# Kernel optimization log

Measured on AMD Instinct MI355X. Metric: run time of the kernel, lower is better.

Reference implementation:

```python
import jax, jax.numpy as jnp
import numpy as np

N_PATHS, SEQ_LEN = 8192, 512
DATA_DIM, HIDDEN = 2, 128
MIN_VOL, MAX_VOL = 1e-4, 5.0


def setup_inputs() -> dict:
    key = jax.random.key(0)
    ks = jax.random.split(key, 10)
    def w(k, fin, fout, scale=1.0):
        return (jax.random.normal(k, (fin, fout), jnp.float32) * (scale / np.sqrt(fin))).astype(jnp.float32)
    # diffusion output bias init from the torch module: log(exp(target_vol) - 1 + 1e-8)
    gb3_init = float(np.log(np.exp(0.1) - 1.0 + 1e-8))
    return {
        "y0": jax.random.normal(ks[0], (N_PATHS, DATA_DIM), jnp.float32) * 0.1,
        "ts": jnp.arange(SEQ_LEN, dtype=jnp.float32),  # dt = 1.0 between outputs
        "dW": jax.random.normal(ks[1], (SEQ_LEN - 1, N_PATHS, DATA_DIM), jnp.float32),
        "fw1": w(ks[2], DATA_DIM + 1, HIDDEN), "fb1": jnp.zeros((HIDDEN,), jnp.float32),
        "fw2": w(ks[3], HIDDEN, HIDDEN),       "fb2": jnp.zeros((HIDDEN,), jnp.float32),
        "fw3": w(ks[4], HIDDEN, DATA_DIM, 0.02), "fb3": jnp.zeros((DATA_DIM,), jnp.float32),
        "gw1": w(ks[5], DATA_DIM, HIDDEN),     "gb1": jnp.zeros((HIDDEN,), jnp.float32),
        "gw2": w(ks[6], HIDDEN, HIDDEN),       "gb2": jnp.zeros((HIDDEN,), jnp.float32),
        "gw3": w(ks[7], HIDDEN, DATA_DIM, 0.02),
        "gb3": jnp.full((DATA_DIM,), gb3_init, jnp.float32),
    }


def _sde_paths(y0, ts, dW, fw1, fb1, fw2, fb2, fw3, fb3, gw1, gb1, gw2, gb2, gw3, gb3):
    def drift(y):  # f(t, y): MLP on [y, spread]
        spread = y[:, 0:1] - y[:, 1:2]
        h = jnp.concatenate([y, spread], axis=-1)            # [N, D+1]
        h = jax.nn.silu(h @ fw1 + fb1)
        h = jax.nn.silu(h @ fw2 + fb2)
        return h @ fw3 + fb3                                  # [N, D]

    def diffusion(y):  # g(t, y): softplus + clamp
        h = jax.nn.silu(y @ gw1 + gb1)
        h = jax.nn.silu(h @ gw2 + gb2)
        raw = h @ gw3 + gb3
        return jnp.clip(jax.nn.softplus(raw), MIN_VOL, MAX_VOL)  # [N, D]

    dts = ts[1:] - ts[:-1]  # [T-1]

    def step(y, inp):
        dw_std, dt = inp
        dw = dw_std * jnp.sqrt(dt)                 # Brownian increment ~ N(0, dt)
        f = drift(y)
        g, vjp_g = jax.vjp(diffusion, y)
        v = 0.5 * (dw * dw - dt)                   # Milstein weight (Ito)
        corr = vjp_g(v * g)[0]                     # torchsde autograd gdg_prod
        y1 = y + f * dt + g * dw + corr
        return y1, y1

    _, ys = jax.lax.scan(step, y0, (dW, dts))      # ys: [T-1, N, D]
    paths = jnp.concatenate([y0[None], ys], axis=0)  # [T, N, D]
    return jnp.transpose(paths, (1, 0, 2))           # [N, T, D]


def reference(y0, ts, dW, fw1, fb1, fw2, fb2, fw3, fb3, gw1, gb1, gw2, gb2, gw3, gb3):
    return _sde_paths(y0, ts, dW, fw1, fb1, fw2, fb2, fw3, fb3,
                      gw1, gb1, gw2, gb2, gw3, gb3)
```

## Files before the change

kernel.cpp:

```cpp
#include <hip/hip_runtime.h>
#include <math.h>

#define H      128
#define NPATH  8192
#define TLEN   512
#define BP     32
#define NTHR   512

typedef short bf16x8 __attribute__((ext_vector_type(8)));
typedef float f32x4  __attribute__((ext_vector_type(4)));

#define MFMA(a,b,c) __builtin_amdgcn_mfma_f32_16x16x32_bf16((a),(b),(c),0,0,0)

#define O_WF2T  0
#define O_WG2T  (O_WF2T + 32768)
#define O_WG2R  (O_WG2T + 32768)
#define O_BFH   (O_WG2R + 32768)
#define O_BFL   (O_BFH + 8192)
#define O_BGH   (O_BFL + 8192)
#define O_BGL   (O_BGH + 8192)
#define O_PF    (O_BGL + 8192)
#define O_PRAW  (O_PF   + 1024)
#define O_PCORR (O_PRAW + 1024)
#define O_TS    (O_PCORR+ 1024)
#define SMEM_BYTES (O_TS + TLEN*4)

__device__ __forceinline__ float bf2f(unsigned v){ return __uint_as_float(v << 16); }
__device__ __forceinline__ unsigned short f2bf(float f){
  unsigned u = __float_as_uint(f);
  return (unsigned short)((u + 0x7fffu + ((u >> 16) & 1u)) >> 16);
}
__device__ __forceinline__ float ldany(const void* p, long long i, bool isbf){
  return isbf ? bf2f(((const unsigned short*)p)[i]) : ((const float*)p)[i];
}
__device__ __forceinline__ unsigned short ldbf(const void* p, long long i, bool isbf){
  return isbf ? ((const unsigned short*)p)[i] : f2bf(((const float*)p)[i]);
}
__device__ __forceinline__ float fsig(float x){
  return __builtin_amdgcn_rcpf(1.0f + __expf(-x));
}
__device__ __forceinline__ float fsilu(float x){ return x * fsig(x); }
__device__ __forceinline__ float fsilud(float x){
  float s = fsig(x); return s * (1.0f + x * (1.0f - s));
}
__device__ __forceinline__ float fsoftplus(float x){
  if (x > 15.0f) return x;
  return __logf(1.0f + __expf(x));
}
__device__ __forceinline__ void split2(float x, unsigned short& hi, unsigned short& lo){
  unsigned short h = f2bf(x);
  hi = h;
  lo = f2bf(x - bf2f(h));
}
__device__ __forceinline__ int physB(int row, int col){
  return (row << 8) + ((((col >> 3) ^ (row & 15)) << 4) | ((col & 7) << 1));
}
__device__ __forceinline__ bf16x8 ldfrag(const char* base, int row, int col){
  union { uint4 u; bf16x8 b; } v;
  v.u = *(const uint4*)(base + physB(row, col));
  return v.b;
}
__device__ __forceinline__ void st8(char* base, int row, int col, const unsigned short h[8]){
  uint4 u = make_uint4((unsigned)h[0] | ((unsigned)h[1] << 16),
                       (unsigned)h[2] | ((unsigned)h[3] << 16),
                       (unsigned)h[4] | ((unsigned)h[5] << 16),
                       (unsigned)h[6] | ((unsigned)h[7] << 16));
  *(uint4*)(base + physB(row, col)) = u;
}
__device__ __forceinline__ void st4(char* base, int row, int col, const unsigned short h[4]){
  uint2 u = make_uint2((unsigned)h[0] | ((unsigned)h[1] << 16),
                       (unsigned)h[2] | ((unsigned)h[3] << 16));
  *(uint2*)(base + physB(row, col)) = u;
}

__global__ __launch_bounds__(NTHR, 2)
void GeneratorSDE_kernel(const void* __restrict__ y0, const void* __restrict__ ts,
                         const void* __restrict__ dW,
                         const void* __restrict__ fw1, const void* __restrict__ fb1,
                         const void* __restrict__ fw2, const void* __restrict__ fb2,
                         const void* __restrict__ fw3, const void* __restrict__ fb3,
                         const void* __restrict__ gw1, const void* __restrict__ gb1,
                         const void* __restrict__ gw2, const void* __restrict__ gb2,
                         const void* __restrict__ gw3, const void* __restrict__ gb3,
                         void* __restrict__ out)
{
  extern __shared__ char sm[];
  const int tid  = threadIdx.x;
  const int lane = tid & 63;
  const int w    = tid >> 6;
  const int wp   = w >> 1;
  const int nt   = w & 1;
  const int m16  = lane & 15;
  const int q    = lane >> 4;
  const int gpb  = blockIdx.x * BP;
  const int p1   = nt*16 + m16;
  const int gp   = gpb + p1;
  const int k8   = wp*32 + q*8;

  const bool isbf = (((const unsigned*)ts)[1] != 0x3f800000u);

  for (int e = tid; e < H * H; e += NTHR){
    int k = e >> 7, n = e & 127;
    unsigned short fv = ldbf(fw2, e, isbf);
    unsigned short gv = ldbf(gw2, e, isbf);
    *(unsigned short*)(sm + O_WF2T + physB(n, k)) = fv;
    *(unsigned short*)(sm + O_WG2T + physB(n, k)) = gv;
    *(unsigned short*)(sm + O_WG2R + physB(k, n)) = gv;
  }
  for (int e = tid; e < TLEN; e += NTHR)
    ((float*)(sm + O_TS))[e] = ldany(ts, e, isbf);

  float w3f0[8], w3f1[8], w3g0[8], w3g1[8], gw1b0[8], gw1b1[8], gb1b[8], fb2r[8], gb2r[8];
  #pragma unroll
  for (int i = 0; i < 8; ++i){
    int nr = 32*wp + ((i >> 2) << 4) + (q << 2) + (i & 3);
    w3f0[i]  = ldany(fw3, 2*nr + 0, isbf);
    w3f1[i]  = ldany(fw3, 2*nr + 1, isbf);
    w3g0[i]  = ldany(gw3, 2*nr + 0, isbf);
    w3g1[i]  = ldany(gw3, 2*nr + 1, isbf);
    gw1b0[i] = ldany(gw1, nr,       isbf);
    gw1b1[i] = ldany(gw1, H + nr,   isbf);
    gb1b[i]  = ldany(gb1, nr,       isbf);
    fb2r[i]  = ldany(fb2, nr,       isbf);
    gb2r[i]  = ldany(gb2, nr,       isbf);
  }
  float fw1r0[8], fw1r1[8], fw1r2[8], fb1r[8], gw1r0[8], gw1r1[8], gb1r[8];
  #pragma unroll
  for (int kk = 0; kk < 8; ++kk){
    int k = k8 + kk;
    fw1r0[kk] = ldany(fw1, k,       isbf);
    fw1r1[kk] = ldany(fw1, H + k,   isbf);
    fw1r2[kk] = ldany(fw1, 2*H + k, isbf);
    fb1r[kk]  = ldany(fb1, k,       isbf);
    gw1r0[kk] = ldany(gw1, k,       isbf);
    gw1r1[kk] = ldany(gw1, H + k,   isbf);
    gb1r[kk]  = ldany(gb1, k,       isbf);
  }
  const float fb3r0 = ldany(fb3, 0, isbf), fb3r1 = ldany(fb3, 1, isbf);
  const float gb3r0 = ldany(gb3, 0, isbf), gb3r1 = ldany(gb3, 1, isbf);

  float ycur0 = ldany(y0, (long long)gp*2 + 0, isbf);
  float ycur1 = ldany(y0, (long long)gp*2 + 1, isbf);
  if (w < 2 && lane < 16){
    size_t r = (size_t)gp * TLEN;
    if (isbf) ((unsigned*)out)[r] = (unsigned)f2bf(ycur0) | ((unsigned)f2bf(ycur1) << 16);
    else      ((float2*)out)[r]   = make_float2(ycur0, ycur1);
  }
  float2 dwcur;
  {
    long long e = (long long)gp * 2;
    if (isbf){ unsigned u = *(const unsigned*)((const unsigned short*)dW + e);
               dwcur = make_float2(bf2f(u & 0xffffu), bf2f(u >> 16)); }
    else       dwcur = *(const float2*)((const float*)dW + e);
  }
  __syncthreads();

  const float* TSf = (const float*)(sm + O_TS);

  for (int t = 0; t < TLEN - 1; ++t){
    float dt = TSf[t+1] - TSf[t];
    float sqdt = sqrtf(dt);

    float2 dwnext;
    {
      int tn = (t + 1 <= TLEN - 2) ? t + 1 : TLEN - 2;
      long long e = ((long long)tn * NPATH + gp) * 2;
      if (isbf){ unsigned u = *(const unsigned*)((const unsigned short*)dW + e);
                 dwnext = make_float2(bf2f(u & 0xffffu), bf2f(u >> 16)); }
      else       dwnext = *(const float2*)((const float*)dW + e);
    }

    {
      float ysp = ycur0 - ycur1;
      unsigned short fh[8], fl[8], gh[8], gl[8];
      #pragma unroll
      for (int kk = 0; kk < 8; ++kk){
        float hf = fsilu(fb1r[kk] + ycur0*fw1r0[kk] + ycur1*fw1r1[kk] + ysp*fw1r2[kk]);
        float hg = fsilu(gb1r[kk] + ycur0*gw1r0[kk] + ycur1*gw1r1[kk]);
        split2(hf, fh[kk], fl[kk]);
        split2(hg, gh[kk], gl[kk]);
      }
      st8(sm + O_BFH, p1, k8, fh);
      st8(sm + O_BFL, p1, k8, fl);
      st8(sm + O_BGH, p1, k8, gh);
      st8(sm + O_BGL, p1, k8, gl);
    }
    __syncthreads();

    f32x4 accg[2];
    {
      f32x4 accf[2];
      accf[0] = (f32x4)0.f; accf[1] = (f32x4)0.f;
      accg[0] = (f32x4)0.f; accg[1] = (f32x4)0.f;
      #pragma unroll
      for (int kt = 0; kt < 4; ++kt){
        int colk = kt*32 + q*8;
        bf16x8 af0 = ldfrag(sm + O_WF2T, 32*wp + m16,      colk);
        bf16x8 af1 = ldfrag(sm + O_WF2T, 32*wp + 16 + m16, colk);
        bf16x8 bfh = ldfrag(sm + O_BFH, p1, colk);
        bf16x8 bfl = ldfrag(sm + O_BFL, p1, colk);
        accf[0] = MFMA(af0, bfl, accf[0]); accf[0] = MFMA(af0, bfh, accf[0]);
        accf[1] = MFMA(af1, bfl, accf[1]); accf[1] = MFMA(af1, bfh, accf[1]);
        bf16x8 ag0 = ldfrag(sm + O_WG2T, 32*wp + m16,      colk);
        bf16x8 ag1 = ldfrag(sm + O_WG2T, 32*wp + 16 + m16, colk);
        bf16x8 bgh = ldfrag(sm + O_BGH, p1, colk);
        bf16x8 bgl = ldfrag(sm + O_BGL, p1, colk);
        accg[0] = MFMA(ag0, bgl, accg[0]); accg[0] = MFMA(ag0, bgh, accg[0]);
        accg[1] = MFMA(ag1, bgl, accg[1]); accg[1] = MFMA(ag1, bgh, accg[1]);
      }
      float pf0 = 0, pf1 = 0, pr0 = 0, pr1 = 0;
      #pragma unroll
      for (int mi = 0; mi < 2; ++mi)
        #pragma unroll
        for (int r = 0; r < 4; ++r){
          int i = mi*4 + r;
          float vf = fsilu(accf[mi][r] + fb2r[i]);
          pf0 += vf * w3f0[i];
          pf1 += vf * w3f1[i];
          float zg = accg[mi][r] + gb2r[i];
          accg[mi][r] = zg;
          float vg = fsilu(zg);
          pr0 += vg * w3g0[i];
          pr1 += vg * w3g1[i];
        }
      pf0 += __shfl_xor(pf0, 16, 64); pf0 += __shfl_xor(pf0, 32, 64);
      pf1 += __shfl_xor(pf1, 16, 64); pf1 += __shfl_xor(pf1, 32, 64);
      pr0 += __shfl_xor(pr0, 16, 64); pr0 += __shfl_xor(pr0, 32, 64);
      pr1 += __shfl_xor(pr1, 16, 64); pr1 += __shfl_xor(pr1, 32, 64);
      if (lane < 16){
        *(float2*)(sm + O_PF   + (wp*32 + p1)*8) = make_float2(pf0, pf1);
        *(float2*)(sm + O_PRAW + (wp*32 + p1)*8) = make_float2(pr0, pr1);
      }
    }
    __syncthreads();

    float g0, g1, dw0, dw1, cr0, cr1;
    {
      float raw0 = gb3r0, raw1 = gb3r1;
      #pragma unroll
      for (int w2 = 0; w2 < 4; ++w2){
        float2 v = *(const float2*)(sm + O_PRAW + (w2*32 + p1)*8);
        raw0 += v.x; raw1 += v.y;
      }
      dw0 = dwcur.x * sqdt; dw1 = dwcur.y * sqdt;
      float vv0 = 0.5f*(dw0*dw0 - dt), vv1 = 0.5f*(dw1*dw1 - dt);
      float sp0 = fsoftplus(raw0), sp1 = fsoftplus(raw1);
      g0 = fminf(fmaxf(sp0, 1e-4f), 5.0f);
      g1 = fminf(fmaxf(sp1, 1e-4f), 5.0f);
      float m0 = (sp0 > 1e-4f && sp0 < 5.0f) ? 1.0f : 0.0f;
      float m1 = (sp1 > 1e-4f && sp1 < 5.0f) ? 1.0f : 0.0f;
      cr0 = vv0 * (g0 * fsig(raw0) * m0);
      cr1 = vv1 * (g1 * fsig(raw1) * m1);
    }

    #pragma unroll
    for (int mi = 0; mi < 2; ++mi){
      unsigned short hi[4], lo[4];
      #pragma unroll
      for (int r = 0; r < 4; ++r){
        int i = mi*4 + r;
        float c2 = (cr0 * w3g0[i] + cr1 * w3g1[i]) * fsilud(accg[mi][r]);
        split2(c2, hi[r], lo[r]);
      }
      st4(sm + O_BFH, p1, 32*wp + 16*mi + q*4, hi);
      st4(sm + O_BFL, p1, 32*wp + 16*mi + q*4, lo);
    }
    __syncthreads();

    {
      f32x4 accc[2];
      accc[0] = (f32x4)0.f; accc[1] = (f32x4)0.f;
      #pragma unroll
      for (int kt = 0; kt < 4; ++kt){
        int colk = kt*32 + q*8;
        bf16x8 a0 = ldfrag(sm + O_WG2R, 32*wp + m16,      colk);
        bf16x8 a1 = ldfrag(sm + O_WG2R, 32*wp + 16 + m16, colk);
        bf16x8 bh = ldfrag(sm + O_BFH, p1, colk);
        bf16x8 bl = ldfrag(sm + O_BFL, p1, colk);
        accc[0] = MFMA(a0, bl, accc[0]); accc[0] = MFMA(a0, bh, accc[0]);
        accc[1] = MFMA(a1, bl, accc[1]); accc[1] = MFMA(a1, bh, accc[1]);
      }
      float pc0 = 0, pc1 = 0;
      #pragma unroll
      for (int mi = 0; mi < 2; ++mi)
        #pragma unroll
        for (int r = 0; r < 4; ++r){
          int i = mi*4 + r;
          float z1 = gb1b[i] + ycur0*gw1b0[i] + ycur1*gw1b1[i];
          float u  = accc[mi][r] * fsilud(z1);
          pc0 += u * gw1b0[i];
          pc1 += u * gw1b1[i];
        }
      pc0 += __shfl_xor(pc0, 16, 64); pc0 += __shfl_xor(pc0, 32, 64);
      pc1 += __shfl_xor(pc1, 16, 64); pc1 += __shfl_xor(pc1, 32, 64);
      if (lane < 16)
        *(float2*)(sm + O_PCORR + (wp*32 + p1)*8) = make_float2(pc0, pc1);
    }
    __syncthreads();

    {
      float f0 = fb3r0, f1 = fb3r1, c0 = 0.f, c1 = 0.f;
      #pragma unroll
      for (int w2 = 0; w2 < 4; ++w2){
        float2 a = *(const float2*)(sm + O_PF    + (w2*32 + p1)*8);
        float2 b = *(const float2*)(sm + O_PCORR + (w2*32 + p1)*8);
        f0 += a.x; f1 += a.y; c0 += b.x; c1 += b.y;
      }
      ycur0 += f0*dt + g0*dw0 + c0;
      ycur1 += f1*dt + g1*dw1 + c1;
      if (w < 2 && lane < 16){
        size_t r = (size_t)gp * TLEN + (t + 1);
        if (isbf) ((unsigned*)out)[r] = (unsigned)f2bf(ycur0) | ((unsigned)f2bf(ycur1) << 16);
        else      ((float2*)out)[r]   = make_float2(ycur0, ycur1);
      }
      dwcur = dwnext;
    }
  }
}

extern "C" void kernel_launch(void* const* d_in, const int* in_sizes, int n_in,
                              void* d_out, int out_size, void* d_ws, size_t ws_size,
                              hipStream_t stream)
{
  (void)in_sizes; (void)n_in; (void)out_size; (void)d_ws; (void)ws_size;
  hipFuncSetAttribute((const void*)GeneratorSDE_kernel,
                      hipFuncAttributeMaxDynamicSharedMemorySize, SMEM_BYTES);
  GeneratorSDE_kernel<<<dim3(NPATH / BP), dim3(NTHR), SMEM_BYTES, stream>>>(
      d_in[0], d_in[1], d_in[2],
      d_in[3], d_in[4], d_in[5], d_in[6], d_in[7], d_in[8],
      d_in[9], d_in[10], d_in[11], d_in[12], d_in[13], d_in[14],
      d_out);
}
```

Measured before the change: 2.066 ms.

## Software-pipeline two path halves across phases with register-resident weight fragments

Splits each block's 32 paths into two 16-path halves and interleaves their per-step phases, so the MFMA work of one half overlaps the elementwise work of the other. Each of the 8 waves now owns a 16-row slice of the hidden dimension, which lets the layer-2 weight fragments be loaded into registers once instead of re-read from LDS every step. The layer-1 work is split across waves by network (drift or diffusion), and the bf16 hi/lo split now uses truncation with packed stores. The price is more register pressure, a trickier cross-half schedule, and truncation instead of round-to-nearest for the hi part.

```diff
diff --git a/kernel.cpp b/kernel.cpp
--- a/kernel.cpp
+++ b/kernel.cpp
@@ -13,16 +13,16 @@
 #define MFMA(a,b,c) __builtin_amdgcn_mfma_f32_16x16x32_bf16((a),(b),(c),0,0,0)
 
 #define O_WF2T  0
-#define O_WG2T  (O_WF2T + 32768)
-#define O_WG2R  (O_WG2T + 32768)
-#define O_BFH   (O_WG2R + 32768)
-#define O_BFL   (O_BFH + 8192)
-#define O_BGH   (O_BFL + 8192)
-#define O_BGL   (O_BGH + 8192)
-#define O_PF    (O_BGL + 8192)
-#define O_PRAW  (O_PF   + 1024)
-#define O_PCORR (O_PRAW + 1024)
-#define O_TS    (O_PCORR+ 1024)
+#define O_WG2T  32768
+#define O_WG2R  65536
+#define O_BFH   98304
+#define O_BFL   106496
+#define O_BGH   114688
+#define O_BGL   122880
+#define O_PF    131072
+#define O_PRAW  133120
+#define O_PCORR 135168
+#define O_TS    137216
 #define SMEM_BYTES (O_TS + TLEN*4)
 
 __device__ __forceinline__ float bf2f(unsigned v){ return __uint_as_float(v << 16); }
@@ -47,10 +47,13 @@
   if (x > 15.0f) return x;
   return __logf(1.0f + __expf(x));
 }
-__device__ __forceinline__ void split2(float x, unsigned short& hi, unsigned short& lo){
-  unsigned short h = f2bf(x);
-  hi = h;
-  lo = f2bf(x - bf2f(h));
+__device__ __forceinline__ void splitpk(float x0, float x1, unsigned& hipk, unsigned& lopk){
+  unsigned u0 = __float_as_uint(x0), u1 = __float_as_uint(x1);
+  unsigned h0 = u0 & 0xffff0000u, h1 = u1 & 0xffff0000u;
+  hipk = (u0 >> 16) | h1;
+  float l0 = x0 - __uint_as_float(h0);
+  float l1 = x1 - __uint_as_float(h1);
+  lopk = (__float_as_uint(l0) >> 16) | (__float_as_uint(l1) & 0xffff0000u);
 }
 __device__ __forceinline__ int physB(int row, int col){
   return (row << 8) + ((((col >> 3) ^ (row & 15)) << 4) | ((col & 7) << 1));
@@ -59,18 +62,6 @@
   union { uint4 u; bf16x8 b; } v;
   v.u = *(const uint4*)(base + physB(row, col));
   return v.b;
-}
-__device__ __forceinline__ void st8(char* base, int row, int col, const unsigned short h[8]){
-  uint4 u = make_uint4((unsigned)h[0] | ((unsigned)h[1] << 16),
-                       (unsigned)h[2] | ((unsigned)h[3] << 16),
-                       (unsigned)h[4] | ((unsigned)h[5] << 16),
-                       (unsigned)h[6] | ((unsigned)h[7] << 16));
-  *(uint4*)(base + physB(row, col)) = u;
-}
-__device__ __forceinline__ void st4(char* base, int row, int col, const unsigned short h[4]){
-  uint2 u = make_uint2((unsigned)h[0] | ((unsigned)h[1] << 16),
-                       (unsigned)h[2] | ((unsigned)h[3] << 16));
-  *(uint2*)(base + physB(row, col)) = u;
 }
 
 __global__ __launch_bounds__(NTHR, 2)
@@ -88,14 +79,11 @@
   const int tid  = threadIdx.x;
   const int lane = tid & 63;
   const int w    = tid >> 6;
-  const int wp   = w >> 1;
-  const int nt   = w & 1;
   const int m16  = lane & 15;
   const int q    = lane >> 4;
   const int gpb  = blockIdx.x * BP;
-  const int p1   = nt*16 + m16;
-  const int gp   = gpb + p1;
-  const int k8   = wp*32 + q*8;
+  const int net  = w & 1;
+  const int k8   = (w >> 1)*32 + q*8;
 
   const bool isbf = (((const unsigned*)ts)[1] != 0x3f800000u);
 
@@ -110,211 +98,221 @@
   for (int e = tid; e < TLEN; e += NTHR)
     ((float*)(sm + O_TS))[e] = ldany(ts, e, isbf);
 
-  float w3f0[8], w3f1[8], w3g0[8], w3g1[8], gw1b0[8], gw1b1[8], gb1b[8], fb2r[8], gb2r[8];
-  #pragma unroll
-  for (int i = 0; i < 8; ++i){
-    int nr = 32*wp + ((i >> 2) << 4) + (q << 2) + (i & 3);
-    w3f0[i]  = ldany(fw3, 2*nr + 0, isbf);
-    w3f1[i]  = ldany(fw3, 2*nr + 1, isbf);
-    w3g0[i]  = ldany(gw3, 2*nr + 0, isbf);
-    w3g1[i]  = ldany(gw3, 2*nr + 1, isbf);
-    gw1b0[i] = ldany(gw1, nr,       isbf);
-    gw1b1[i] = ldany(gw1, H + nr,   isbf);
-    gb1b[i]  = ldany(gb1, nr,       isbf);
-    fb2r[i]  = ldany(fb2, nr,       isbf);
-    gb2r[i]  = ldany(gb2, nr,       isbf);
-  }
-  float fw1r0[8], fw1r1[8], fw1r2[8], fb1r[8], gw1r0[8], gw1r1[8], gb1r[8];
+  float w3f0[4], w3f1[4], w3g0[4], w3g1[4], fb2r[4], gb2r[4], gw1b0[4], gw1b1[4], gb1b[4];
+  #pragma unroll
+  for (int r = 0; r < 4; ++r){
+    int nr = 16*w + (q << 2) + r;
+    w3f0[r]  = ldany(fw3, 2*nr + 0, isbf);
+    w3f1[r]  = ldany(fw3, 2*nr + 1, isbf);
+    w3g0[r]  = ldany(gw3, 2*nr + 0, isbf);
+    w3g1[r]  = ldany(gw3, 2*nr + 1, isbf);
+    gw1b0[r] = ldany(gw1, nr,       isbf);
+    gw1b1[r] = ldany(gw1, H + nr,   isbf);
+    gb1b[r]  = ldany(gb1, nr,       isbf);
+    fb2r[r]  = ldany(fb2, nr,       isbf);
+    gb2r[r]  = ldany(gb2, nr,       isbf);
+  }
+  float wr0[8], wr1[8], wr2[8], brg[8];
   #pragma unroll
   for (int kk = 0; kk < 8; ++kk){
     int k = k8 + kk;
-    fw1r0[kk] = ldany(fw1, k,       isbf);
-    fw1r1[kk] = ldany(fw1, H + k,   isbf);
-    fw1r2[kk] = ldany(fw1, 2*H + k, isbf);
-    fb1r[kk]  = ldany(fb1, k,       isbf);
-    gw1r0[kk] = ldany(gw1, k,       isbf);
-    gw1r1[kk] = ldany(gw1, H + k,   isbf);
-    gb1r[kk]  = ldany(gb1, k,       isbf);
+    if (net == 0){
+      wr0[kk] = ldany(fw1, k,       isbf);
+      wr1[kk] = ldany(fw1, H + k,   isbf);
+      wr2[kk] = ldany(fw1, 2*H + k, isbf);
+      brg[kk] = ldany(fb1, k,       isbf);
+    } else {
+      wr0[kk] = ldany(gw1, k,       isbf);
+      wr1[kk] = ldany(gw1, H + k,   isbf);
+      wr2[kk] = 0.0f;
+      brg[kk] = ldany(gb1, k,       isbf);
+    }
   }
   const float fb3r0 = ldany(fb3, 0, isbf), fb3r1 = ldany(fb3, 1, isbf);
   const float gb3r0 = ldany(gb3, 0, isbf), gb3r1 = ldany(gb3, 1, isbf);
 
-  float ycur0 = ldany(y0, (long long)gp*2 + 0, isbf);
-  float ycur1 = ldany(y0, (long long)gp*2 + 1, isbf);
-  if (w < 2 && lane < 16){
-    size_t r = (size_t)gp * TLEN;
-    if (isbf) ((unsigned*)out)[r] = (unsigned)f2bf(ycur0) | ((unsigned)f2bf(ycur1) << 16);
-    else      ((float2*)out)[r]   = make_float2(ycur0, ycur1);
-  }
-  float2 dwcur;
-  {
+  float2 yc[2], dwc[2], dwn[2], gS[2], dwS[2];
+  f32x4  az[2];
+  #pragma unroll
+  for (int h = 0; h < 2; ++h){
+    int gp = gpb + 16*h + m16;
+    yc[h].x = ldany(y0, (long long)gp*2 + 0, isbf);
+    yc[h].y = ldany(y0, (long long)gp*2 + 1, isbf);
     long long e = (long long)gp * 2;
     if (isbf){ unsigned u = *(const unsigned*)((const unsigned short*)dW + e);
-               dwcur = make_float2(bf2f(u & 0xffffu), bf2f(u >> 16)); }
-    else       dwcur = *(const float2*)((const float*)dW + e);
+               dwc[h] = make_float2(bf2f(u & 0xffffu), bf2f(u >> 16)); }
+    else       dwc[h] = *(const float2*)((const float*)dW + e);
+    dwn[h] = dwc[h]; gS[h] = make_float2(0.f,0.f); dwS[h] = make_float2(0.f,0.f);
+    az[h] = (f32x4)0.f;
+  }
+  #pragma unroll
+  for (int h = 0; h < 2; ++h){
+    if (w == h && lane < 16){
+      size_t r = (size_t)(gpb + 16*h + lane) * TLEN;
+      if (isbf) ((unsigned*)out)[r] = (unsigned)f2bf(yc[h].x) | ((unsigned)f2bf(yc[h].y) << 16);
+      else      ((float2*)out)[r]   = make_float2(yc[h].x, yc[h].y);
+    }
   }
   __syncthreads();
 
+  bf16x8 afr[4], agr[4], abr[4];
+  #pragma unroll
+  for (int kt = 0; kt < 4; ++kt){
+    int colk = kt*32 + q*8;
+    afr[kt] = ldfrag(sm + O_WF2T, 16*w + m16, colk);
+    agr[kt] = ldfrag(sm + O_WG2T, 16*w + m16, colk);
+    abr[kt] = ldfrag(sm + O_WG2R, 16*w + m16, colk);
+  }
+
   const float* TSf = (const float*)(sm + O_TS);
-
-  for (int t = 0; t < TLEN - 1; ++t){
-    float dt = TSf[t+1] - TSf[t];
-    float sqdt = sqrtf(dt);
-
-    float2 dwnext;
-    {
-      int tn = (t + 1 <= TLEN - 2) ? t + 1 : TLEN - 2;
-      long long e = ((long long)tn * NPATH + gp) * 2;
-      if (isbf){ unsigned u = *(const unsigned*)((const unsigned short*)dW + e);
-                 dwnext = make_float2(bf2f(u & 0xffffu), bf2f(u >> 16)); }
-      else       dwnext = *(const float2*)((const float*)dW + e);
-    }
-
-    {
-      float ysp = ycur0 - ycur1;
-      unsigned short fh[8], fl[8], gh[8], gl[8];
-      #pragma unroll
-      for (int kk = 0; kk < 8; ++kk){
-        float hf = fsilu(fb1r[kk] + ycur0*fw1r0[kk] + ycur1*fw1r1[kk] + ysp*fw1r2[kk]);
-        float hg = fsilu(gb1r[kk] + ycur0*gw1r0[kk] + ycur1*gw1r1[kk]);
-        split2(hf, fh[kk], fl[kk]);
-        split2(hg, gh[kk], gl[kk]);
-      }
-      st8(sm + O_BFH, p1, k8, fh);
-      st8(sm + O_BFL, p1, k8, fl);
-      st8(sm + O_BGH, p1, k8, gh);
-      st8(sm + O_BGL, p1, k8, gl);
-    }
-    __syncthreads();
-
-    f32x4 accg[2];
-    {
-      f32x4 accf[2];
-      accf[0] = (f32x4)0.f; accf[1] = (f32x4)0.f;
-      accg[0] = (f32x4)0.f; accg[1] = (f32x4)0.f;
-      #pragma unroll
-      for (int kt = 0; kt < 4; ++kt){
-        int colk = kt*32 + q*8;
-        bf16x8 af0 = ldfrag(sm + O_WF2T, 32*wp + m16,      colk);
-        bf16x8 af1 = ldfrag(sm + O_WF2T, 32*wp + 16 + m16, colk);
-        bf16x8 bfh = ldfrag(sm + O_BFH, p1, colk);
-        bf16x8 bfl = ldfrag(sm + O_BFL, p1, colk);
-        accf[0] = MFMA(af0, bfl, accf[0]); accf[0] = MFMA(af0, bfh, accf[0]);
-        accf[1] = MFMA(af1, bfl, accf[1]); accf[1] = MFMA(af1, bfh, accf[1]);
-        bf16x8 ag0 = ldfrag(sm + O_WG2T, 32*wp + m16,      colk);
-        bf16x8 ag1 = ldfrag(sm + O_WG2T, 32*wp + 16 + m16, colk);
-        bf16x8 bgh = ldfrag(sm + O_BGH, p1, colk);
-        bf16x8 bgl = ldfrag(sm + O_BGL, p1, colk);
-        accg[0] = MFMA(ag0, bgl, accg[0]); accg[0] = MFMA(ag0, bgh, accg[0]);
-        accg[1] = MFMA(ag1, bgl, accg[1]); accg[1] = MFMA(ag1, bgh, accg[1]);
-      }
-      float pf0 = 0, pf1 = 0, pr0 = 0, pr1 = 0;
-      #pragma unroll
-      for (int mi = 0; mi < 2; ++mi)
-        #pragma unroll
-        for (int r = 0; r < 4; ++r){
-          int i = mi*4 + r;
-          float vf = fsilu(accf[mi][r] + fb2r[i]);
-          pf0 += vf * w3f0[i];
-          pf1 += vf * w3f1[i];
-          float zg = accg[mi][r] + gb2r[i];
-          accg[mi][r] = zg;
-          float vg = fsilu(zg);
-          pr0 += vg * w3g0[i];
-          pr1 += vg * w3g1[i];
-        }
-      pf0 += __shfl_xor(pf0, 16, 64); pf0 += __shfl_xor(pf0, 32, 64);
-      pf1 += __shfl_xor(pf1, 16, 64); pf1 += __shfl_xor(pf1, 32, 64);
-      pr0 += __shfl_xor(pr0, 16, 64); pr0 += __shfl_xor(pr0, 32, 64);
-      pr1 += __shfl_xor(pr1, 16, 64); pr1 += __shfl_xor(pr1, 32, 64);
-      if (lane < 16){
-        *(float2*)(sm + O_PF   + (wp*32 + p1)*8) = make_float2(pf0, pf1);
-        *(float2*)(sm + O_PRAW + (wp*32 + p1)*8) = make_float2(pr0, pr1);
-      }
-    }
-    __syncthreads();
-
-    float g0, g1, dw0, dw1, cr0, cr1;
-    {
-      float raw0 = gb3r0, raw1 = gb3r1;
-      #pragma unroll
-      for (int w2 = 0; w2 < 4; ++w2){
-        float2 v = *(const float2*)(sm + O_PRAW + (w2*32 + p1)*8);
-        raw0 += v.x; raw1 += v.y;
-      }
-      dw0 = dwcur.x * sqdt; dw1 = dwcur.y * sqdt;
-      float vv0 = 0.5f*(dw0*dw0 - dt), vv1 = 0.5f*(dw1*dw1 - dt);
-      float sp0 = fsoftplus(raw0), sp1 = fsoftplus(raw1);
-      g0 = fminf(fmaxf(sp0, 1e-4f), 5.0f);
-      g1 = fminf(fmaxf(sp1, 1e-4f), 5.0f);
-      float m0 = (sp0 > 1e-4f && sp0 < 5.0f) ? 1.0f : 0.0f;
-      float m1 = (sp1 > 1e-4f && sp1 < 5.0f) ? 1.0f : 0.0f;
-      cr0 = vv0 * (g0 * fsig(raw0) * m0);
-      cr1 = vv1 * (g1 * fsig(raw1) * m1);
-    }
-
-    #pragma unroll
-    for (int mi = 0; mi < 2; ++mi){
-      unsigned short hi[4], lo[4];
-      #pragma unroll
-      for (int r = 0; r < 4; ++r){
-        int i = mi*4 + r;
-        float c2 = (cr0 * w3g0[i] + cr1 * w3g1[i]) * fsilud(accg[mi][r]);
-        split2(c2, hi[r], lo[r]);
-      }
-      st4(sm + O_BFH, p1, 32*wp + 16*mi + q*4, hi);
-      st4(sm + O_BFL, p1, 32*wp + 16*mi + q*4, lo);
-    }
-    __syncthreads();
-
-    {
-      f32x4 accc[2];
-      accc[0] = (f32x4)0.f; accc[1] = (f32x4)0.f;
-      #pragma unroll
-      for (int kt = 0; kt < 4; ++kt){
-        int colk = kt*32 + q*8;
-        bf16x8 a0 = ldfrag(sm + O_WG2R, 32*wp + m16,      colk);
-        bf16x8 a1 = ldfrag(sm + O_WG2R, 32*wp + 16 + m16, colk);
-        bf16x8 bh = ldfrag(sm + O_BFH, p1, colk);
-        bf16x8 bl = ldfrag(sm + O_BFL, p1, colk);
-        accc[0] = MFMA(a0, bl, accc[0]); accc[0] = MFMA(a0, bh, accc[0]);
-        accc[1] = MFMA(a1, bl, accc[1]); accc[1] = MFMA(a1, bh, accc[1]);
-      }
-      float pc0 = 0, pc1 = 0;
-      #pragma unroll
-      for (int mi = 0; mi < 2; ++mi)
-        #pragma unroll
-        for (int r = 0; r < 4; ++r){
-          int i = mi*4 + r;
-          float z1 = gb1b[i] + ycur0*gw1b0[i] + ycur1*gw1b1[i];
-          float u  = accc[mi][r] * fsilud(z1);
-          pc0 += u * gw1b0[i];
-          pc1 += u * gw1b1[i];
-        }
-      pc0 += __shfl_xor(pc0, 16, 64); pc0 += __shfl_xor(pc0, 32, 64);
-      pc1 += __shfl_xor(pc1, 16, 64); pc1 += __shfl_xor(pc1, 32, 64);
-      if (lane < 16)
-        *(float2*)(sm + O_PCORR + (wp*32 + p1)*8) = make_float2(pc0, pc1);
-    }
-    __syncthreads();
-
-    {
+  float dtprev = 1.0f, dtcur = 1.0f, sqcur = 1.0f;
+
+  auto P0 = [&](int h, int c){
+    if (c > 0){
       float f0 = fb3r0, f1 = fb3r1, c0 = 0.f, c1 = 0.f;
       #pragma unroll
-      for (int w2 = 0; w2 < 4; ++w2){
-        float2 a = *(const float2*)(sm + O_PF    + (w2*32 + p1)*8);
-        float2 b = *(const float2*)(sm + O_PCORR + (w2*32 + p1)*8);
+      for (int w2 = 0; w2 < 8; ++w2){
+        float2 a = *(const float2*)(sm + O_PF    + (w2*32 + 16*h + m16)*8);
+        float2 b = *(const float2*)(sm + O_PCORR + (w2*32 + 16*h + m16)*8);
         f0 += a.x; f1 += a.y; c0 += b.x; c1 += b.y;
       }
-      ycur0 += f0*dt + g0*dw0 + c0;
-      ycur1 += f1*dt + g1*dw1 + c1;
-      if (w < 2 && lane < 16){
-        size_t r = (size_t)gp * TLEN + (t + 1);
-        if (isbf) ((unsigned*)out)[r] = (unsigned)f2bf(ycur0) | ((unsigned)f2bf(ycur1) << 16);
-        else      ((float2*)out)[r]   = make_float2(ycur0, ycur1);
+      yc[h].x += f0*dtprev + gS[h].x*dwS[h].x + c0;
+      yc[h].y += f1*dtprev + gS[h].y*dwS[h].y + c1;
+      if (w == h && lane < 16){
+        size_t r = (size_t)(gpb + 16*h + lane) * TLEN + c;
+        if (isbf) ((unsigned*)out)[r] = (unsigned)f2bf(yc[h].x) | ((unsigned)f2bf(yc[h].y) << 16);
+        else      ((float2*)out)[r]   = make_float2(yc[h].x, yc[h].y);
       }
-      dwcur = dwnext;
-    }
+    }
+    if (c < TLEN - 1){
+      int tn = (c + 1 <= TLEN - 2) ? c + 1 : TLEN - 2;
+      long long e = ((long long)tn * NPATH + (gpb + 16*h + m16)) * 2;
+      if (isbf){ unsigned u = *(const unsigned*)((const unsigned short*)dW + e);
+                 dwn[h] = make_float2(bf2f(u & 0xffffu), bf2f(u >> 16)); }
+      else       dwn[h] = *(const float2*)((const float*)dW + e);
+
+      float ya = yc[h].x, yb = yc[h].y, ysp = ya - yb;
+      float v[8];
+      #pragma unroll
+      for (int kk = 0; kk < 8; ++kk)
+        v[kk] = fsilu(brg[kk] + ya*wr0[kk] + yb*wr1[kk] + ysp*wr2[kk]);
+      unsigned hp[4], lp[4];
+      splitpk(v[0], v[1], hp[0], lp[0]);
+      splitpk(v[2], v[3], hp[1], lp[1]);
+      splitpk(v[4], v[5], hp[2], lp[2]);
+      splitpk(v[6], v[7], hp[3], lp[3]);
+      char* bh = sm + (net ? O_BGH : O_BFH);
+      char* bl = sm + (net ? O_BGL : O_BFL);
+      int off = physB(16*h + m16, k8);
+      *(uint4*)(bh + off) = make_uint4(hp[0], hp[1], hp[2], hp[3]);
+      *(uint4*)(bl + off) = make_uint4(lp[0], lp[1], lp[2], lp[3]);
+    }
+  };
+
+  auto P1 = [&](int h){
+    f32x4 acf = (f32x4)0.f, acg = (f32x4)0.f;
+    const int rA = 16*h + m16;
+    #pragma unroll
+    for (int kt = 0; kt < 4; ++kt){
+      int colk = kt*32 + q*8;
+      bf16x8 xfh = ldfrag(sm + O_BFH, rA, colk);
+      bf16x8 xfl = ldfrag(sm + O_BFL, rA, colk);
+      acf = MFMA(afr[kt], xfl, acf);
+      acf = MFMA(afr[kt], xfh, acf);
+      bf16x8 xgh = ldfrag(sm + O_BGH, rA, colk);
+      bf16x8 xgl = ldfrag(sm + O_BGL, rA, colk);
+      acg = MFMA(agr[kt], xgl, acg);
+      acg = MFMA(agr[kt], xgh, acg);
+    }
+    float pf0 = 0, pf1 = 0, pr0 = 0, pr1 = 0;
+    #pragma unroll
+    for (int r = 0; r < 4; ++r){
+      float vf = fsilu(acf[r] + fb2r[r]);
+      pf0 += vf * w3f0[r]; pf1 += vf * w3f1[r];
+      float zg = acg[r] + gb2r[r];
+      acg[r] = zg;
+      float vg = fsilu(zg);
+      pr0 += vg * w3g0[r]; pr1 += vg * w3g1[r];
+    }
+    az[h] = acg;
+    pf0 += __shfl_xor(pf0, 16, 64); pf0 += __shfl_xor(pf0, 32, 64);
+    pf1 += __shfl_xor(pf1, 16, 64); pf1 += __shfl_xor(pf1, 32, 64);
+    pr0 += __shfl_xor(pr0, 16, 64); pr0 += __shfl_xor(pr0, 32, 64);
+    pr1 += __shfl_xor(pr1, 16, 64); pr1 += __shfl_xor(pr1, 32, 64);
+    if (lane < 16){
+      *(float2*)(sm + O_PF   + (w*32 + 16*h + lane)*8) = make_float2(pf0, pf1);
+      *(float2*)(sm + O_PRAW + (w*32 + 16*h + lane)*8) = make_float2(pr0, pr1);
+    }
+  };
+
+  auto P2 = [&](int h){
+    float raw0 = gb3r0, raw1 = gb3r1;
+    #pragma unroll
+    for (int w2 = 0; w2 < 8; ++w2){
+      float2 v = *(const float2*)(sm + O_PRAW + (w2*32 + 16*h + m16)*8);
+      raw0 += v.x; raw1 += v.y;
+    }
+    float dw0 = dwc[h].x * sqcur, dw1 = dwc[h].y * sqcur;
+    float vv0 = 0.5f*(dw0*dw0 - dtcur), vv1 = 0.5f*(dw1*dw1 - dtcur);
+    float sp0 = fsoftplus(raw0), sp1 = fsoftplus(raw1);
+    float g0 = fminf(fmaxf(sp0, 1e-4f), 5.0f);
+    float g1 = fminf(fmaxf(sp1, 1e-4f), 5.0f);
+    float m0 = (sp0 > 1e-4f && sp0 < 5.0f) ? 1.0f : 0.0f;
+    float m1 = (sp1 > 1e-4f && sp1 < 5.0f) ? 1.0f : 0.0f;
+    float cr0 = vv0 * (g0 * fsig(raw0) * m0);
+    float cr1 = vv1 * (g1 * fsig(raw1) * m1);
+    gS[h]  = make_float2(g0, g1);
+    dwS[h] = make_float2(dw0, dw1);
+    dwc[h] = dwn[h];
+    float c2v[4];
+    #pragma unroll
+    for (int r = 0; r < 4; ++r)
+      c2v[r] = (cr0 * w3g0[r] + cr1 * w3g1[r]) * fsilud(az[h][r]);
+    unsigned hp0, lp0, hp1, lp1;
+    splitpk(c2v[0], c2v[1], hp0, lp0);
+    splitpk(c2v[2], c2v[3], hp1, lp1);
+    int off = physB(16*h + m16, 16*w + q*4);
+    *(uint2*)(sm + O_BFH + off) = make_uint2(hp0, hp1);
+    *(uint2*)(sm + O_BFL + off) = make_uint2(lp0, lp1);
+  };
+
+  auto P3 = [&](int h){
+    f32x4 acc = (f32x4)0.f;
+    const int rB = 16*h + m16;
+    #pragma unroll
+    for (int kt = 0; kt < 4; ++kt){
+      int colk = kt*32 + q*8;
+      bf16x8 xh = ldfrag(sm + O_BFH, rB, colk);
+      bf16x8 xl = ldfrag(sm + O_BFL, rB, colk);
+      acc = MFMA(abr[kt], xl, acc);
+      acc = MFMA(abr[kt], xh, acc);
+    }
+    float pc0 = 0, pc1 = 0;
+    #pragma unroll
+    for (int r = 0; r < 4; ++r){
+      float z1 = gb1b[r] + yc[h].x*gw1b0[r] + yc[h].y*gw1b1[r];
+      float u  = acc[r] * fsilud(z1);
+      pc0 += u * gw1b0[r]; pc1 += u * gw1b1[r];
+    }
+    pc0 += __shfl_xor(pc0, 16, 64); pc0 += __shfl_xor(pc0, 32, 64);
+    pc1 += __shfl_xor(pc1, 16, 64); pc1 += __shfl_xor(pc1, 32, 64);
+    if (lane < 16)
+      *(float2*)(sm + O_PCORR + (w*32 + 16*h + lane)*8) = make_float2(pc0, pc1);
+  };
+
+  for (int c = 0; c <= TLEN - 1; ++c){
+    if (c < TLEN - 1){ dtcur = TSf[c+1] - TSf[c]; sqcur = sqrtf(dtcur); }
+    P0(0, c);
+    if (c > 0) P3(1);
+    __syncthreads();
+    if (c < TLEN - 1) P1(0);
+    P0(1, c);
+    __syncthreads();
+    if (c < TLEN - 1){ P2(0); P1(1); }
+    __syncthreads();
+    if (c < TLEN - 1){ P3(0); P2(1); }
+    __syncthreads();
+    dtprev = dtcur;
   }
 }
 
```

Result: slower. 2.693 ms (+30.4%).
